# Kernel optimization log

Measured on AMD Instinct MI355X. Metric: run time of the kernel, lower is better.

The kernel has to match this reference:

```python
import jax, jax.numpy as jnp
import numpy as np

N = 50000      # total nodes
G = 100        # graphs in batch
NPG = N // G   # nodes per graph (contiguous)
E = 800000     # total edges (avg degree 16)
F_IN = 256
HID = 128
C = 4


def setup_inputs() -> dict:
    key = jax.random.key(0)
    ks = jax.random.split(key, 16)
    w = lambda k, shape: (jax.random.normal(k, shape, dtype=jnp.float32) * 0.02)
    x = jax.random.normal(ks[0], (N, F_IN), dtype=jnp.float32)
    # edges within graphs: pick a graph per edge, then local src/dst
    g = jax.random.randint(ks[1], (E,), 0, G, dtype=jnp.int32)
    src = g * NPG + jax.random.randint(ks[2], (E,), 0, NPG, dtype=jnp.int32)
    dst = g * NPG + jax.random.randint(ks[3], (E,), 0, NPG, dtype=jnp.int32)
    edge_index = jnp.stack([src, dst], axis=0)
    batch = jnp.repeat(jnp.arange(G, dtype=jnp.int32), NPG)
    return {
        "x": x,
        "edge_index": edge_index,
        "batch": batch,
        "num_graphs": G,
        "W_bu1": w(ks[4], (F_IN, HID)), "b_bu1": jnp.zeros((HID,), jnp.float32),
        "W_td1": w(ks[5], (F_IN, HID)), "b_td1": jnp.zeros((HID,), jnp.float32),
        "W_bu2": w(ks[6], (F_IN + HID, HID)), "b_bu2": jnp.zeros((HID,), jnp.float32),
        "W_td2": w(ks[7], (F_IN + HID, HID)), "b_td2": jnp.zeros((HID,), jnp.float32),
        "W_lin": w(ks[8], (2 * HID, C)), "b_lin": jnp.zeros((C,), jnp.float32),
    }


def _gcn(h_in, src, dst, W, b, n):
    """PyG GCNConv: sym-normalized aggregation with self loops, then bias."""
    h = h_in @ W                                        # [N, H]
    # deg = in-degree at dst + 1 (self loop)
    deg = jnp.ones((n,), h.dtype).at[dst].add(jnp.ones(src.shape, h.dtype))
    dinv = jax.lax.rsqrt(deg)                           # [N]
    coef = (dinv[src] * dinv[dst])[:, None]             # [E, 1]
    agg = jnp.zeros_like(h).at[dst].add(h[src] * coef)  # scatter-add messages
    agg = agg + h * (dinv * dinv)[:, None]              # self-loop term
    return agg + b


def reference(x, edge_index, batch, num_graphs,
              W_bu1, b_bu1, W_td1, b_td1,
              W_bu2, b_bu2, W_td2, b_td2,
              W_lin, b_lin):
    n = x.shape[0]
    g = num_graphs
    src, dst = edge_index[0], edge_index[1]  # top-down direction
    # root = first node index of each (contiguous) graph
    root = jax.ops.segment_min(jnp.arange(n), batch, num_segments=g)  # [G]
    root_full = x[root][batch]                                        # repeat_interleave of root feats
    # layer 1: bottom-up uses flipped edges, top-down uses edges as-is
    l1_bu = _gcn(x, dst, src, W_bu1, b_bu1, n)
    l1_td = _gcn(x, src, dst, W_td1, b_td1, n)
    cb = jax.nn.relu(jnp.concatenate([root_full, l1_bu], axis=-1))  # dropout is identity in eval
    ct = jax.nn.relu(jnp.concatenate([root_full, l1_td], axis=-1))
    # layer 2: original code passes the top-down edge_index to BOTH convs
    l2_bu = jax.nn.relu(_gcn(cb, src, dst, W_bu2, b_bu2, n))
    l2_td = jax.nn.relu(_gcn(ct, src, dst, W_td2, b_td2, n))
    # repeat root rows over each graph then segment-mean == the root row itself
    pb = l2_bu[root]   # [G, HID]
    pt = l2_td[root]   # [G, HID]
    total = jnp.concatenate([pb, pt], axis=-1)          # [G, 2*HID]
    return jax.nn.log_softmax(total @ W_lin + b_lin, axis=-1)
```

## Files before the change

kernel.cpp:

```cpp
#include <hip/hip_runtime.h>
#include <hip/hip_bf16.h>
#include <math.h>

constexpr int F_IN = 256;
constexpr int HID  = 128;
constexpr int CLS  = 4;

constexpr int SMAX  = 2560;
constexpr int ECAP  = 64;
constexpr int QCAP  = 512;
constexpr int GMAX  = 128;

__global__ void k_init(int* __restrict__ sidx, int* __restrict__ slist,
                       int* __restrict__ counters, int G, int NPG) {
  int g = threadIdx.x + blockIdx.x * blockDim.x;
  if (g == 0) counters[0] = G;
  if (g < G) { sidx[g * NPG] = g; slist[g] = g * NPG; }
}

__global__ void k_claim(const int* __restrict__ src, const int* __restrict__ dst,
                        int* __restrict__ sidx, int* __restrict__ slist,
                        int* __restrict__ qbuf, int* __restrict__ qcur,
                        int* __restrict__ counters, int E, int NPG) {
  int i = blockIdx.x * blockDim.x + threadIdx.x;
  int e0 = i * 4;
  int dv[4];
  int ne = 0;
  if (e0 + 3 < E) {
    int4 d4 = ((const int4*)dst)[i];
    dv[0] = d4.x; dv[1] = d4.y; dv[2] = d4.z; dv[3] = d4.w;
    ne = 4;
  } else {
    for (int e = e0; e < E; ++e) dv[ne++] = dst[e];
  }
#pragma unroll
  for (int k = 0; k < 4; ++k) {
    if (k >= ne) break;
    int d = dv[k];
    int dg = d / NPG;
    if (d - dg * NPG == 0) {
      int s = src[e0 + k];
      int p = atomicAdd(&qcur[dg], 1);
      if (p < QCAP) qbuf[dg * QCAP + p] = s;
      if (atomicCAS(&sidx[s], -1, -2) == -1) {
        int slot = atomicAdd(&counters[0], 1);
        if (slot < SMAX) { slist[slot] = s; sidx[s] = slot; }
        else sidx[s] = -1;
      }
    }
  }
}

__global__ void k_degfill(const int* __restrict__ src, const int* __restrict__ dst,
                          const int* __restrict__ sidx,
                          int* __restrict__ cnt_bu, int* __restrict__ cnt_td,
                          int* __restrict__ cur_bu, int* __restrict__ cur_td,
                          int* __restrict__ ebuf_bu, int* __restrict__ ebuf_td, int E) {
  int i = blockIdx.x * blockDim.x + threadIdx.x;
  int e0 = i * 4;
  int sv[4], dv[4];
  int ne = 0;
  if (e0 + 3 < E) {
    int4 s4 = ((const int4*)src)[i];
    int4 d4 = ((const int4*)dst)[i];
    sv[0] = s4.x; sv[1] = s4.y; sv[2] = s4.z; sv[3] = s4.w;
    dv[0] = d4.x; dv[1] = d4.y; dv[2] = d4.z; dv[3] = d4.w;
    ne = 4;
  } else {
    for (int e = e0; e < E; ++e) { sv[ne] = src[e]; dv[ne] = dst[e]; ++ne; }
  }
#pragma unroll
  for (int k = 0; k < 4; ++k) {
    if (k >= ne) break;
    int s = sv[k], d = dv[k];
    atomicAdd(&cnt_bu[s], 1);
    atomicAdd(&cnt_td[d], 1);
    int ss = sidx[s];
    if (ss >= 0) { int p = atomicAdd(&cur_bu[ss], 1); if (p < ECAP) ebuf_bu[ss * ECAP + p] = d; }
    int sd = sidx[d];
    if (sd >= 0) { int p = atomicAdd(&cur_td[sd], 1); if (p < ECAP) ebuf_td[sd * ECAP + p] = s; }
  }
}

__global__ void k_gather(const float* __restrict__ x, const int* __restrict__ slist,
                         const int* __restrict__ counters,
                         const int* __restrict__ cnt_bu, const int* __restrict__ cnt_td,
                         const int* __restrict__ ebuf_bu, const int* __restrict__ ebuf_td,
                         float* __restrict__ zbu, float* __restrict__ ztd) {
  int scnt = min(counters[0], SMAX);
  int lane = threadIdx.x & 63;
  int w = (blockIdx.x * blockDim.x + threadIdx.x) >> 6;
  bool td = (w >= SMAX);
  int slot = td ? w - SMAX : w;
  if (slot >= scnt) return;
  const int* cnt = td ? cnt_td : cnt_bu;
  const int* eb  = (td ? ebuf_td : ebuf_bu) + slot * ECAP;
  int u = slist[slot];
  int deg = min(cnt[u], ECAP);
  float ax = 0.f, ay = 0.f, az = 0.f, aw = 0.f;
  for (int j = 0; j < deg; ++j) {
    int node = eb[j];
    float dv = rsqrtf(1.f + (float)cnt[node]);
    float4 v = ((const float4*)x)[(size_t)node * 64 + lane];
    ax += dv * v.x; ay += dv * v.y; az += dv * v.z; aw += dv * v.w;
  }
  float du = rsqrtf(1.f + (float)cnt[u]);
  float4 xv = ((const float4*)x)[(size_t)u * 64 + lane];
  float4 r;
  r.x = du * ax + du * du * xv.x;
  r.y = du * ay + du * du * xv.y;
  r.z = du * az + du * du * xv.z;
  r.w = du * aw + du * du * xv.w;
  ((float4*)(td ? ztd : zbu))[(size_t)slot * 64 + lane] = r;
}

__global__ void k_l1(const int* __restrict__ counters,
                     const float* __restrict__ zbu, const float* __restrict__ ztd,
                     const float* __restrict__ Wbu, const float* __restrict__ bbu,
                     const float* __restrict__ Wtd, const float* __restrict__ btd,
                     float* __restrict__ l1_bu, float* __restrict__ l1_td) {
  constexpr int TS = 8;
  __shared__ float zb[TS][F_IN];
  __shared__ float zt[TS][F_IN];
  int scnt = min(counters[0], SMAX);
  int base = blockIdx.x * TS;
  if (base >= scnt) return;
  int nslots = min(TS, scnt - base);
  int tid = threadIdx.x;
  for (int t = 0; t < nslots; ++t) {
    zb[t][tid] = zbu[(size_t)(base + t) * F_IN + tid];
    zt[t][tid] = ztd[(size_t)(base + t) * F_IN + tid];
  }
  __syncthreads();
  bool isbu = (tid < HID);
  int h = isbu ? tid : tid - HID;
  const float* W = isbu ? Wbu : Wtd;
  float acc[TS];
#pragma unroll
  for (int t = 0; t < TS; ++t) acc[t] = 0.f;
  for (int f = 0; f < F_IN; ++f) {
    float wv = W[f * HID + h];
#pragma unroll
    for (int t = 0; t < TS; ++t) acc[t] += (isbu ? zb[t][f] : zt[t][f]) * wv;
  }
  float bias = isbu ? bbu[h] : btd[h];
  float* outp = isbu ? l1_bu : l1_td;
  for (int t = 0; t < nslots; ++t)
    outp[(size_t)(base + t) * HID + h] = acc[t] + bias;
}

__global__ void k_out(const float* __restrict__ x,
                      const int* __restrict__ sidx, const int* __restrict__ cnt_td,
                      const int* __restrict__ qbuf, const int* __restrict__ qcur,
                      const float* __restrict__ l1_bu, const float* __restrict__ l1_td,
                      const float* __restrict__ Wbu2, const float* __restrict__ bbu2,
                      const float* __restrict__ Wtd2, const float* __restrict__ btd2,
                      const float* __restrict__ Wlin, const float* __restrict__ blin,
                      float* __restrict__ out, int G, int NPG) {
  __shared__ int   s_slot[QCAP + 1];
  __shared__ float s_coef[QCAP + 1];
  __shared__ float front[F_IN];
  __shared__ float av[2 * HID];
  __shared__ float total[2 * HID];
  __shared__ float logits[CLS];
  int g = blockIdx.x;
  int tid = threadIdx.x;
  int r = g * NPG;
  int nq = min(qcur[g], QCAP);
  int items = nq + 1;
  float dr = rsqrtf(1.f + (float)cnt_td[r]);
  for (int i = tid; i < items; i += 256) {
    int s = (i < nq) ? qbuf[g * QCAP + i] : r;
    s_slot[i] = sidx[s];
    s_coef[i] = rsqrtf(1.f + (float)cnt_td[s]) * dr;
  }
  __syncthreads();
  bool isbu = (tid < HID);
  int h = isbu ? tid : tid - HID;
  const float* l1v = isbu ? l1_bu : l1_td;
  float acc = 0.f, csum = 0.f;
  for (int i = 0; i < items; ++i) {
    float c = s_coef[i];
    csum += c;
    int slot = s_slot[i];
    if (slot >= 0) acc += c * fmaxf(l1v[(size_t)slot * HID + h], 0.f);
  }
  av[tid]    = acc;
  front[tid] = csum * fmaxf(x[(size_t)r * F_IN + tid], 0.f);
  __syncthreads();
  const float* W  = isbu ? Wbu2 : Wtd2;
  const float* ah = isbu ? av : (av + HID);
  float acc2 = isbu ? bbu2[h] : btd2[h];
  for (int f = 0; f < F_IN; ++f) acc2 += front[f] * W[f * HID + h];
  for (int j = 0; j < HID; ++j)  acc2 += ah[j] * W[(F_IN + j) * HID + h];
  total[tid] = fmaxf(acc2, 0.f);
  __syncthreads();
  if (tid < CLS) {
    float a = blin[tid];
    for (int k = 0; k < 2 * HID; ++k) a += total[k] * Wlin[k * CLS + tid];
    logits[tid] = a;
  }
  __syncthreads();
  if (tid < CLS) {
    float m = logits[0];
    for (int c = 1; c < CLS; ++c) m = fmaxf(m, logits[c]);
    float se = 0.f;
    for (int c = 0; c < CLS; ++c) se += expf(logits[c] - m);
    out[(size_t)g * CLS + tid] = logits[tid] - m - logf(se);
  }
}

extern "C" void kernel_launch(void* const* d_in, const int* in_sizes, int n_in,
                              void* d_out, int out_size, void* d_ws, size_t ws_size,
                              hipStream_t stream) {
  const float* x    = (const float*)d_in[0];
  const int*  eidx  = (const int*)d_in[1];
  const float* Wbu1 = (const float*)d_in[4];
  const float* bbu1 = (const float*)d_in[5];
  const float* Wtd1 = (const float*)d_in[6];
  const float* btd1 = (const float*)d_in[7];
  const float* Wbu2 = (const float*)d_in[8];
  const float* bbu2 = (const float*)d_in[9];
  const float* Wtd2 = (const float*)d_in[10];
  const float* btd2 = (const float*)d_in[11];
  const float* Wlin = (const float*)d_in[12];
  const float* blin = (const float*)d_in[13];
  float* out = (float*)d_out;

  int N = in_sizes[2];
  int E = in_sizes[1] / 2;
  int G = out_size / CLS;
  int NPG = N / G;
  const int* src = eidx;
  const int* dst = eidx + E;

  char* p = (char*)d_ws;
  auto alloc = [&](size_t bytes) -> char* {
    char* r = p; p += (bytes + 255) & ~(size_t)255; return r;
  };
  int*   counters  = (int*)  alloc(64);
  int*   cnt_bu    = (int*)  alloc((size_t)N * 4);
  int*   cnt_td    = (int*)  alloc((size_t)N * 4);
  int*   qcur      = (int*)  alloc((size_t)GMAX * 4);
  int*   cur_bu    = (int*)  alloc((size_t)SMAX * 4);
  int*   cur_td    = (int*)  alloc((size_t)SMAX * 4);
  size_t zero_bytes = (size_t)(p - (char*)d_ws);
  int*   sidx      = (int*)  alloc((size_t)N * 4);
  int*   slist     = (int*)  alloc((size_t)SMAX * 4);
  int*   qbuf      = (int*)  alloc((size_t)GMAX * QCAP * 4);
  int*   ebuf_bu   = (int*)  alloc((size_t)SMAX * ECAP * 4);
  int*   ebuf_td   = (int*)  alloc((size_t)SMAX * ECAP * 4);
  float* zbu       = (float*)alloc((size_t)SMAX * F_IN * 4);
  float* ztd       = (float*)alloc((size_t)SMAX * F_IN * 4);
  float* l1_bu     = (float*)alloc((size_t)SMAX * HID * 4);
  float* l1_td     = (float*)alloc((size_t)SMAX * HID * 4);

  hipMemsetAsync(d_ws, 0, zero_bytes, stream);
  hipMemsetAsync(sidx, 0xFF, (size_t)N * 4, stream);

  const int T = 256;
  int quarter = (E + 3) / 4;
  k_init   <<<1, 128, 0, stream>>>(sidx, slist, counters, G, NPG);
  k_claim  <<<(quarter + T - 1) / T, T, 0, stream>>>(src, dst, sidx, slist,
                                                     qbuf, qcur, counters, E, NPG);
  k_degfill<<<(quarter + T - 1) / T, T, 0, stream>>>(src, dst, sidx,
                                                     cnt_bu, cnt_td, cur_bu, cur_td,
                                                     ebuf_bu, ebuf_td, E);
  k_gather <<<(2 * SMAX * 64 + T - 1) / T, T, 0, stream>>>(x, slist, counters,
                                                     cnt_bu, cnt_td, ebuf_bu, ebuf_td,
                                                     zbu, ztd);
  k_l1     <<<(SMAX + 7) / 8, T, 0, stream>>>(counters, zbu, ztd,
                                              Wbu1, bbu1, Wtd1, btd1, l1_bu, l1_td);
  k_out    <<<G, T, 0, stream>>>(x, sidx, cnt_td, qbuf, qcur,
                                 l1_bu, l1_td, Wbu2, bbu2, Wtd2, btd2,
                                 Wlin, blin, out, G, NPG);
}
```

Baseline: 270.1 us.

## Privatize degree counters per XCD, fuse gather into layer-1 GEMM, drop memsets

Degree counters are replicated per XCD, indexed by the hardware XCC_ID register, and incremented with relaxed workgroup-scope atomics. This is meant to cut contention and cross-die atomic traffic. Readers sum the eight copies, which adds eight loads per degree lookup in the gather and output kernels. The neighbour gather is fused into the layer-1 GEMM kernel, so the z rows go straight to shared memory instead of a global round trip. The two memsets and the init kernel are replaced by a single setup kernel. The workgroup-scope atomics rely on the device performing global atomics at L2 to stay correct across workgroups.

```diff
diff --git a/kernel.cpp b/kernel.cpp
--- a/kernel.cpp
+++ b/kernel.cpp
@@ -1,5 +1,4 @@
 #include <hip/hip_runtime.h>
-#include <hip/hip_bf16.h>
 #include <math.h>
 
 constexpr int F_IN = 256;
@@ -10,12 +9,37 @@
 constexpr int ECAP  = 64;
 constexpr int QCAP  = 512;
 constexpr int GMAX  = 128;
-
-__global__ void k_init(int* __restrict__ sidx, int* __restrict__ slist,
-                       int* __restrict__ counters, int G, int NPG) {
-  int g = threadIdx.x + blockIdx.x * blockDim.x;
-  if (g == 0) counters[0] = G;
-  if (g < G) { sidx[g * NPG] = g; slist[g] = g * NPG; }
+constexpr int NXCD  = 8;
+
+__device__ __forceinline__ int xcc_id() {
+  int x;
+  asm volatile("s_getreg_b32 %0, hwreg(HW_REG_XCC_ID)" : "=s"(x));
+  return x & (NXCD - 1);
+}
+
+__device__ __forceinline__ int degsum(const int* __restrict__ cnt, int N, int v) {
+  int d = 0;
+#pragma unroll
+  for (int k = 0; k < NXCD; ++k) d += cnt[k * N + v];
+  return d;
+}
+
+__global__ void k_setup(int* __restrict__ sidx, int* __restrict__ slist,
+                        int* __restrict__ counters,
+                        int* __restrict__ cnt_bu, int* __restrict__ cnt_td,
+                        int* __restrict__ qcur, int* __restrict__ cur_bu,
+                        int* __restrict__ cur_td, int N, int G, int NPG) {
+  int i = blockIdx.x * blockDim.x + threadIdx.x;
+  if (i == 0) counters[0] = G;
+  if (i < GMAX) qcur[i] = 0;
+  if (i < SMAX) { cur_bu[i] = 0; cur_td[i] = 0; }
+  if (i >= N) return;
+#pragma unroll
+  for (int k = 0; k < NXCD; ++k) { cnt_bu[k * N + i] = 0; cnt_td[k * N + i] = 0; }
+  int g = i / NPG;
+  bool isroot = (i - g * NPG) == 0;
+  sidx[i] = isroot ? g : -1;
+  if (isroot) slist[g] = i;
 }
 
 __global__ void k_claim(const int* __restrict__ src, const int* __restrict__ dst,
@@ -55,7 +79,11 @@
                           const int* __restrict__ sidx,
                           int* __restrict__ cnt_bu, int* __restrict__ cnt_td,
                           int* __restrict__ cur_bu, int* __restrict__ cur_td,
-                          int* __restrict__ ebuf_bu, int* __restrict__ ebuf_td, int E) {
+                          int* __restrict__ ebuf_bu, int* __restrict__ ebuf_td,
+                          int E, int N) {
+  int xc = xcc_id();
+  int* cb = cnt_bu + xc * N;
+  int* ct = cnt_td + xc * N;
   int i = blockIdx.x * blockDim.x + threadIdx.x;
   int e0 = i * 4;
   int sv[4], dv[4];
@@ -73,8 +101,8 @@
   for (int k = 0; k < 4; ++k) {
     if (k >= ne) break;
     int s = sv[k], d = dv[k];
-    atomicAdd(&cnt_bu[s], 1);
-    atomicAdd(&cnt_td[d], 1);
+    __hip_atomic_fetch_add(&cb[s], 1, __ATOMIC_RELAXED, __HIP_MEMORY_SCOPE_WORKGROUP);
+    __hip_atomic_fetch_add(&ct[d], 1, __ATOMIC_RELAXED, __HIP_MEMORY_SCOPE_WORKGROUP);
     int ss = sidx[s];
     if (ss >= 0) { int p = atomicAdd(&cur_bu[ss], 1); if (p < ECAP) ebuf_bu[ss * ECAP + p] = d; }
     int sd = sidx[d];
@@ -82,54 +110,46 @@
   }
 }
 
-__global__ void k_gather(const float* __restrict__ x, const int* __restrict__ slist,
-                         const int* __restrict__ counters,
-                         const int* __restrict__ cnt_bu, const int* __restrict__ cnt_td,
-                         const int* __restrict__ ebuf_bu, const int* __restrict__ ebuf_td,
-                         float* __restrict__ zbu, float* __restrict__ ztd) {
-  int scnt = min(counters[0], SMAX);
-  int lane = threadIdx.x & 63;
-  int w = (blockIdx.x * blockDim.x + threadIdx.x) >> 6;
-  bool td = (w >= SMAX);
-  int slot = td ? w - SMAX : w;
-  if (slot >= scnt) return;
-  const int* cnt = td ? cnt_td : cnt_bu;
-  const int* eb  = (td ? ebuf_td : ebuf_bu) + slot * ECAP;
-  int u = slist[slot];
-  int deg = min(cnt[u], ECAP);
-  float ax = 0.f, ay = 0.f, az = 0.f, aw = 0.f;
-  for (int j = 0; j < deg; ++j) {
-    int node = eb[j];
-    float dv = rsqrtf(1.f + (float)cnt[node]);
-    float4 v = ((const float4*)x)[(size_t)node * 64 + lane];
-    ax += dv * v.x; ay += dv * v.y; az += dv * v.z; aw += dv * v.w;
-  }
-  float du = rsqrtf(1.f + (float)cnt[u]);
-  float4 xv = ((const float4*)x)[(size_t)u * 64 + lane];
-  float4 r;
-  r.x = du * ax + du * du * xv.x;
-  r.y = du * ay + du * du * xv.y;
-  r.z = du * az + du * du * xv.z;
-  r.w = du * aw + du * du * xv.w;
-  ((float4*)(td ? ztd : zbu))[(size_t)slot * 64 + lane] = r;
-}
-
-__global__ void k_l1(const int* __restrict__ counters,
-                     const float* __restrict__ zbu, const float* __restrict__ ztd,
-                     const float* __restrict__ Wbu, const float* __restrict__ bbu,
-                     const float* __restrict__ Wtd, const float* __restrict__ btd,
-                     float* __restrict__ l1_bu, float* __restrict__ l1_td) {
+__global__ __launch_bounds__(256) void k_gl1(
+    const float* __restrict__ x, const int* __restrict__ slist,
+    const int* __restrict__ counters,
+    const int* __restrict__ cnt_bu, const int* __restrict__ cnt_td,
+    const int* __restrict__ ebuf_bu, const int* __restrict__ ebuf_td,
+    const float* __restrict__ Wbu, const float* __restrict__ bbu,
+    const float* __restrict__ Wtd, const float* __restrict__ btd,
+    float* __restrict__ l1_bu, float* __restrict__ l1_td, int N) {
   constexpr int TS = 8;
   __shared__ float zb[TS][F_IN];
   __shared__ float zt[TS][F_IN];
   int scnt = min(counters[0], SMAX);
   int base = blockIdx.x * TS;
   if (base >= scnt) return;
-  int nslots = min(TS, scnt - base);
-  int tid = threadIdx.x;
-  for (int t = 0; t < nslots; ++t) {
-    zb[t][tid] = zbu[(size_t)(base + t) * F_IN + tid];
-    zt[t][tid] = ztd[(size_t)(base + t) * F_IN + tid];
+  int ns = min(TS, scnt - base);
+  int tid = threadIdx.x, lane = tid & 63, wv = tid >> 6;
+  for (int q = 0; q < 4; ++q) {
+    int unit = wv * 4 + q;
+    int sl = unit & 7;
+    bool td = unit >= 8;
+    if (sl >= ns) continue;
+    const int* cnt = td ? cnt_td : cnt_bu;
+    const int* eb  = (td ? ebuf_td : ebuf_bu) + (base + sl) * ECAP;
+    int u = slist[base + sl];
+    int dg = degsum(cnt, N, u);
+    int m = min(dg, ECAP);
+    float ax = 0.f, ay = 0.f, az = 0.f, aw = 0.f;
+    for (int j = 0; j < m; ++j) {
+      int node = eb[j];
+      float dv = rsqrtf(1.f + (float)degsum(cnt, N, node));
+      float4 v = ((const float4*)x)[(size_t)node * 64 + lane];
+      ax += dv * v.x; ay += dv * v.y; az += dv * v.z; aw += dv * v.w;
+    }
+    float du = rsqrtf(1.f + (float)dg);
+    float4 xv = ((const float4*)x)[(size_t)u * 64 + lane];
+    float* zrow = td ? zt[sl] : zb[sl];
+    zrow[lane * 4 + 0] = du * ax + du * du * xv.x;
+    zrow[lane * 4 + 1] = du * ay + du * du * xv.y;
+    zrow[lane * 4 + 2] = du * az + du * du * xv.z;
+    zrow[lane * 4 + 3] = du * aw + du * du * xv.w;
   }
   __syncthreads();
   bool isbu = (tid < HID);
@@ -139,13 +159,13 @@
 #pragma unroll
   for (int t = 0; t < TS; ++t) acc[t] = 0.f;
   for (int f = 0; f < F_IN; ++f) {
-    float wv = W[f * HID + h];
-#pragma unroll
-    for (int t = 0; t < TS; ++t) acc[t] += (isbu ? zb[t][f] : zt[t][f]) * wv;
+    float wvv = W[f * HID + h];
+#pragma unroll
+    for (int t = 0; t < TS; ++t) acc[t] += (isbu ? zb[t][f] : zt[t][f]) * wvv;
   }
   float bias = isbu ? bbu[h] : btd[h];
   float* outp = isbu ? l1_bu : l1_td;
-  for (int t = 0; t < nslots; ++t)
+  for (int t = 0; t < ns; ++t)
     outp[(size_t)(base + t) * HID + h] = acc[t] + bias;
 }
 
@@ -156,7 +176,7 @@
                       const float* __restrict__ Wbu2, const float* __restrict__ bbu2,
                       const float* __restrict__ Wtd2, const float* __restrict__ btd2,
                       const float* __restrict__ Wlin, const float* __restrict__ blin,
-                      float* __restrict__ out, int G, int NPG) {
+                      float* __restrict__ out, int G, int NPG, int N) {
   __shared__ int   s_slot[QCAP + 1];
   __shared__ float s_coef[QCAP + 1];
   __shared__ float front[F_IN];
@@ -168,11 +188,11 @@
   int r = g * NPG;
   int nq = min(qcur[g], QCAP);
   int items = nq + 1;
-  float dr = rsqrtf(1.f + (float)cnt_td[r]);
+  float dr = rsqrtf(1.f + (float)degsum(cnt_td, N, r));
   for (int i = tid; i < items; i += 256) {
     int s = (i < nq) ? qbuf[g * QCAP + i] : r;
     s_slot[i] = sidx[s];
-    s_coef[i] = rsqrtf(1.f + (float)cnt_td[s]) * dr;
+    s_coef[i] = rsqrtf(1.f + (float)degsum(cnt_td, N, s)) * dr;
   }
   __syncthreads();
   bool isbu = (tid < HID);
@@ -239,39 +259,33 @@
     char* r = p; p += (bytes + 255) & ~(size_t)255; return r;
   };
   int*   counters  = (int*)  alloc(64);
-  int*   cnt_bu    = (int*)  alloc((size_t)N * 4);
-  int*   cnt_td    = (int*)  alloc((size_t)N * 4);
+  int*   cnt_bu    = (int*)  alloc((size_t)NXCD * N * 4);
+  int*   cnt_td    = (int*)  alloc((size_t)NXCD * N * 4);
   int*   qcur      = (int*)  alloc((size_t)GMAX * 4);
   int*   cur_bu    = (int*)  alloc((size_t)SMAX * 4);
   int*   cur_td    = (int*)  alloc((size_t)SMAX * 4);
-  size_t zero_bytes = (size_t)(p - (char*)d_ws);
   int*   sidx      = (int*)  alloc((size_t)N * 4);
   int*   slist     = (int*)  alloc((size_t)SMAX * 4);
   int*   qbuf      = (int*)  alloc((size_t)GMAX * QCAP * 4);
   int*   ebuf_bu   = (int*)  alloc((size_t)SMAX * ECAP * 4);
   int*   ebuf_td   = (int*)  alloc((size_t)SMAX * ECAP * 4);
-  float* zbu       = (float*)alloc((size_t)SMAX * F_IN * 4);
-  float* ztd       = (float*)alloc((size_t)SMAX * F_IN * 4);
   float* l1_bu     = (float*)alloc((size_t)SMAX * HID * 4);
   float* l1_td     = (float*)alloc((size_t)SMAX * HID * 4);
 
-  hipMemsetAsync(d_ws, 0, zero_bytes, stream);
-  hipMemsetAsync(sidx, 0xFF, (size_t)N * 4, stream);
-
   const int T = 256;
   int quarter = (E + 3) / 4;
-  k_init   <<<1, 128, 0, stream>>>(sidx, slist, counters, G, NPG);
+  k_setup  <<<(N + T - 1) / T, T, 0, stream>>>(sidx, slist, counters,
+                                               cnt_bu, cnt_td, qcur, cur_bu, cur_td,
+                                               N, G, NPG);
   k_claim  <<<(quarter + T - 1) / T, T, 0, stream>>>(src, dst, sidx, slist,
                                                      qbuf, qcur, counters, E, NPG);
   k_degfill<<<(quarter + T - 1) / T, T, 0, stream>>>(src, dst, sidx,
                                                      cnt_bu, cnt_td, cur_bu, cur_td,
-                                                     ebuf_bu, ebuf_td, E);
-  k_gather <<<(2 * SMAX * 64 + T - 1) / T, T, 0, stream>>>(x, slist, counters,
-                                                     cnt_bu, cnt_td, ebuf_bu, ebuf_td,
-                                                     zbu, ztd);
-  k_l1     <<<(SMAX + 7) / 8, T, 0, stream>>>(counters, zbu, ztd,
-                                              Wbu1, bbu1, Wtd1, btd1, l1_bu, l1_td);
+                                                     ebuf_bu, ebuf_td, E, N);
+  k_gl1    <<<(SMAX + 7) / 8, T, 0, stream>>>(x, slist, counters, cnt_bu, cnt_td,
+                                              ebuf_bu, ebuf_td,
+                                              Wbu1, bbu1, Wtd1, btd1, l1_bu, l1_td, N);
   k_out    <<<G, T, 0, stream>>>(x, sidx, cnt_td, qbuf, qcur,
                                  l1_bu, l1_td, Wbu2, bbu2, Wtd2, btd2,
-                                 Wlin, blin, out, G, NPG);
-}
+                                 Wlin, blin, out, G, NPG, N);
+}
```

After: 284.8 us. 5.5% more time.
